# Performance work log

Hardware: AMD Instinct MI355X
Metric: run time of the kernel (lower is better)

The kernel has to match this reference:

```python
import jax, jax.numpy as jnp
import numpy as np

NC = 6            # CPAB tessellation cells (tess_size=6, zero_boundary=True)
DIM = NC - 1      # theta dimension = 5
SIG_LEN = 2048
CHANNELS = 3
BATCH = 256
FC_IN = 64 * 168  # flattened net_part1 output for signal_len=2048
NUM_SCALING = 0   # N in transform_data_ss
EPS_BN = 1e-5


def _cpab_basis():
    """QR null-space basis of the CPAB continuity + zero-boundary constraints.
    Params ordered [a_1,b_1,...,a_NC,b_NC]; v(x)=a_c x + b_c on cell c."""
    nc = NC
    L = np.zeros((nc + 1, 2 * nc))
    for k in range(1, nc):  # continuity at internal knots x_k = k/nc
        xk = k / nc
        L[k - 1, 2 * (k - 1)] = xk
        L[k - 1, 2 * (k - 1) + 1] = 1.0
        L[k - 1, 2 * k] = -xk
        L[k - 1, 2 * k + 1] = -1.0
    L[nc - 1, 1] = 1.0        # v(0) = 0  -> b_1 = 0
    L[nc, 2 * (nc - 1)] = 1.0  # v(1) = 0 -> a_nc + b_nc = 0
    L[nc, 2 * nc - 1] = 1.0
    Q, _ = np.linalg.qr(L.T, mode='complete')
    return np.ascontiguousarray(Q[:, nc + 1:]).astype(np.float32)  # (12, 5)


def _conv1d(x, w, b):
    y = jax.lax.conv_general_dilated(x, w, (1,), 'VALID',
                                     dimension_numbers=('NCH', 'OIH', 'NCH'))
    return y + b[None, :, None]


def _maxpool1d(x, k, s):
    return jax.lax.reduce_window(x, -jnp.inf, jax.lax.max, (1, 1, k), (1, 1, s), 'VALID')


def _bn(x, g, b, m, v):  # eval-mode BatchNorm1d
    return (x - m[None, :, None]) * (g / jnp.sqrt(v + EPS_BN))[None, :, None] + b[None, :, None]


def _integrate(x, A):
    """Exact CPAB 1D flow integration over t=1 with cell-crossing handling.
    x: (B, n) points in [0,1]; A: (B, NC, 2) per-cell (a, b). Monotone
    trajectories cross at most NC-1 boundaries -> fixed NC+1 iterations."""
    a_all, b_all = A[:, :, 0], A[:, :, 1]
    t = jnp.ones_like(x)
    for _ in range(NC + 1):
        c = jnp.clip(jnp.floor(x * NC).astype(jnp.int32), 0, NC - 1)
        a = jnp.take_along_axis(a_all, c, axis=1)
        b = jnp.take_along_axis(b_all, c, axis=1)
        v = a * x + b
        xb = jnp.where(v >= 0, (c + 1).astype(x.dtype) / NC, c.astype(x.dtype) / NC)
        big_a = jnp.abs(a) > 1e-8
        a_s = jnp.where(big_a, a, 1.0)
        z = x + b / a_s        # shifted coord: x(t) = z*exp(a t) - b/a
        zb = xb + b / a_s
        ratio = zb / jnp.where(jnp.abs(z) > 1e-12, z, 1e-12)
        t_exp = jnp.log(jnp.maximum(ratio, 1e-12)) / a_s
        v_s = jnp.where(jnp.abs(v) > 1e-12, v, 1.0)
        t_lin = (xb - x) / v_s
        thit = jnp.where(big_a, t_exp, t_lin)
        valid = (jnp.abs(v) > 1e-12) & (thit > 0) & (jnp.where(big_a, ratio, 1.0) > 0)
        thit = jnp.where(valid, thit, jnp.inf)
        tau = jnp.minimum(t, thit)
        x_new = jnp.where(big_a, z * jnp.exp(a * tau) - (z - x), x + b * tau)
        hit = thit <= t
        nudge = jnp.where(v >= 0, 1e-6, -1e-6)  # push into next cell
        x = jnp.clip(jnp.where(hit, xb + nudge, x_new), 0.0, 1.0)
        t = jnp.maximum(t - tau, 0.0)
    return x


def _interp1d(data, pos):
    """data: (B, L, C); pos: (B, n) in [0,1] -> (B, n, C) linear interpolation."""
    Lw = data.shape[1]
    p = jnp.clip(pos, 0.0, 1.0) * (Lw - 1)
    x0 = jnp.clip(jnp.floor(p).astype(jnp.int32), 0, Lw - 2)
    w = (p - x0.astype(p.dtype))[:, :, None]
    d0 = jnp.take_along_axis(data, x0[:, :, None], axis=1)
    d1 = jnp.take_along_axis(data, (x0 + 1)[:, :, None], axis=1)
    return d0 * (1.0 - w) + d1 * w


def _transform_data_ss(data, theta, basis, outsize, N):
    """CPAB scaling-and-squaring warp of data (B, L, C) by theta (B, DIM)."""
    Bsz = theta.shape[0]
    A = (theta @ basis.T).reshape(Bsz, NC, 2) / (2.0 ** N)
    grid = jnp.linspace(0.0, 1.0, outsize, dtype=data.dtype)
    grid_t = _integrate(jnp.broadcast_to(grid, (Bsz, outsize)), A)
    for _ in range(N):  # squaring: compose the warp with itself
        grid_t = _interp1d(grid_t[:, :, None], grid_t)[:, :, 0]
    return _interp1d(data, grid_t)


def reference(x, conv1_w, conv1_b, bn1_g, bn1_b, bn1_m, bn1_v,
              conv2_w, conv2_b, bn2_g, bn2_b, bn2_m, bn2_v,
              conv3_w, conv3_b, bn3_g, bn3_b, bn3_m, bn3_v,
              fc1_w, fc1_b, fc2_w, fc2_b, fc3_w, fc3_b, fc4_w, fc4_b, basis):
    # localization net (n_recurrence = 1, back_version = True)
    h = jax.nn.relu(_maxpool1d(_bn(_conv1d(x, conv1_w, conv1_b), bn1_g, bn1_b, bn1_m, bn1_v), 3, 2))
    h = jax.nn.relu(_maxpool1d(_bn(_conv1d(h, conv2_w, conv2_b), bn2_g, bn2_b, bn2_m, bn2_v), 3, 3))
    h = jax.nn.relu(_maxpool1d(_bn(_conv1d(h, conv3_w, conv3_b), bn3_g, bn3_b, bn3_m, bn3_v), 3, 2))
    xs = h.reshape(h.shape[0], -1)  # (B, 64*168)
    xs = jax.nn.relu(xs @ fc1_w.T + fc1_b)
    xs = jax.nn.relu(xs @ fc2_w.T + fc2_b)
    xs = jax.nn.relu(xs @ fc3_w.T + fc3_b)
    theta = jnp.tanh(xs @ fc4_w.T + fc4_b)  # (B, 5)
    data = jnp.transpose(x, (0, 2, 1))       # (B, L, C)
    warped = _transform_data_ss(data, theta, basis, SIG_LEN, NUM_SCALING)
    return jnp.transpose(warped, (0, 2, 1))  # (B, C, L)


def setup_inputs() -> dict:
    key = jax.random.key(0)
    ks = jax.random.split(key, 16)
    def nrm(k, shape, scale):
        return (jax.random.normal(k, shape) * scale).astype(jnp.float32)
    inp = {}
    inp['x'] = jax.random.normal(ks[0], (BATCH, CHANNELS, SIG_LEN), dtype=jnp.float32)
    inp['conv1_w'] = nrm(ks[1], (128, CHANNELS, 3), (CHANNELS * 3) ** -0.5)
    inp['conv1_b'] = nrm(ks[2], (128,), 0.01)
    inp['bn1_g'] = jnp.ones((128,), jnp.float32)
    inp['bn1_b'] = jnp.zeros((128,), jnp.float32)
    inp['bn1_m'] = nrm(ks[3], (128,), 0.1)
    inp['bn1_v'] = jnp.ones((128,), jnp.float32)
    inp['conv2_w'] = nrm(ks[4], (64, 128, 5), (128 * 5) ** -0.5)
    inp['conv2_b'] = nrm(ks[5], (64,), 0.01)
    inp['bn2_g'] = jnp.ones((64,), jnp.float32)
    inp['bn2_b'] = jnp.zeros((64,), jnp.float32)
    inp['bn2_m'] = nrm(ks[6], (64,), 0.1)
    inp['bn2_v'] = jnp.ones((64,), jnp.float32)
    inp['conv3_w'] = nrm(ks[7], (64, 64, 3), (64 * 3) ** -0.5)
    inp['conv3_b'] = nrm(ks[8], (64,), 0.01)
    inp['bn3_g'] = jnp.ones((64,), jnp.float32)
    inp['bn3_b'] = jnp.zeros((64,), jnp.float32)
    inp['bn3_m'] = nrm(ks[9], (64,), 0.1)
    inp['bn3_v'] = jnp.ones((64,), jnp.float32)
    inp['fc1_w'] = nrm(ks[10], (48, FC_IN), FC_IN ** -0.5)
    inp['fc1_b'] = jnp.zeros((48,), jnp.float32)
    inp['fc2_w'] = nrm(ks[11], (32, 48), 48 ** -0.5)
    inp['fc2_b'] = jnp.zeros((32,), jnp.float32)
    inp['fc3_w'] = nrm(ks[12], (16, 32), 32 ** -0.5)
    inp['fc3_b'] = jnp.zeros((16,), jnp.float32)
    # near-identity warp head (original zero-inits weight, identity bias)
    inp['fc4_w'] = nrm(ks[13], (DIM, 16), 0.01)
    inp['fc4_b'] = nrm(ks[14], (DIM,), 0.01)
    inp['basis'] = jnp.asarray(_cpab_basis())
    return inp
```

## Files before the change

kernel.cpp:

```cpp
#include <hip/hip_runtime.h>
#include <math.h>

#define BATCH   256
#define SIGLEN  2048
#define L1OUT   1022
#define L2OUT   339
#define L3OUT   168
#define FCIN    10752

#define TP2   16
#define NROW  52
#define H1S   136
#define H1SZ  (NROW*H1S)

#define TU3   28

typedef float f32x2  __attribute__((ext_vector_type(2)));
typedef float f32x4  __attribute__((ext_vector_type(4)));
typedef short s16x8  __attribute__((ext_vector_type(8)));

__device__ __forceinline__ unsigned short f2bf(float f) {
    unsigned int u = __float_as_uint(f);
    return (unsigned short)((u + 0x7fffu + ((u >> 16) & 1u)) >> 16);
}
__device__ __forceinline__ float bf2f(unsigned short h) {
    return __uint_as_float(((unsigned int)h) << 16);
}
__device__ __forceinline__ f32x2 pkfma(f32x2 a, f32x2 b, f32x2 c) {
    f32x2 d;
    asm("v_pk_fma_f32 %0, %1, %2, %3" : "=v"(d) : "v"(a), "v"(b), "v"(c));
    return d;
}

__launch_bounds__(256)
__global__ void prep_kernel(
    const float* __restrict__ conv1_b,
    const float* __restrict__ g1, const float* __restrict__ b1,
    const float* __restrict__ m1, const float* __restrict__ v1,
    const float* __restrict__ conv2_w, const float* __restrict__ conv2_b,
    const float* __restrict__ g2, const float* __restrict__ b2,
    const float* __restrict__ m2, const float* __restrict__ v2,
    const float* __restrict__ conv3_w, const float* __restrict__ conv3_b,
    const float* __restrict__ g3, const float* __restrict__ b3,
    const float* __restrict__ m3, const float* __restrict__ v3,
    const float* __restrict__ fc1_w,
    unsigned short* __restrict__ w2hi, unsigned short* __restrict__ w2lo,
    unsigned short* __restrict__ w3hi, unsigned short* __restrict__ w3lo,
    float* __restrict__ wp1,
    float* __restrict__ so1, float* __restrict__ so2, float* __restrict__ so3)
{
    __shared__ float tl[64 * 169];

    int t   = threadIdx.x;
    int tid = blockIdx.x * 256 + t;
    int stride = gridDim.x * 256;

    if (blockIdx.x < 48) {
        int o = blockIdx.x;
        for (int i = t; i < FCIN; i += 256) {
            int co = i / L3OUT, u = i - co * L3OUT;
            tl[co * 169 + u] = fc1_w[o * FCIN + i];
        }
        __syncthreads();
        for (int i = t; i < FCIN; i += 256) {
            int u = i >> 6, co = i & 63;
            wp1[o * FCIN + i] = tl[co * 169 + u];
        }
    }

    for (int i = tid; i < 64*128*5; i += stride) {
        int co = i / 640; int rr = i - co*640; int ci = rr / 5; int k = rr - ci*5;
        float w = conv2_w[i];
        unsigned short hi = f2bf(w);
        unsigned short lo = f2bf(w - bf2f(hi));
        int dst = ((k*4 + (ci >> 5))*64 + co)*32 + (ci & 31);
        w2hi[dst] = hi;
        w2lo[dst] = lo;
    }
    for (int i = tid; i < 64*64*3; i += stride) {
        int co = i / 192; int r = i - co*192; int ci = r / 3; int k = r - ci*3;
        float w = conv3_w[i];
        unsigned short hi = f2bf(w);
        unsigned short lo = f2bf(w - bf2f(hi));
        int dst = ((k*2 + (ci >> 5))*64 + co)*32 + (ci & 31);
        w3hi[dst] = hi;
        w3lo[dst] = lo;
    }
    if (tid < 128) {
        float s = g1[tid] / sqrtf(v1[tid] + 1e-5f);
        so1[tid]       = s;
        so1[128 + tid] = (conv1_b[tid] - m1[tid]) * s + b1[tid];
    }
    if (tid < 64) {
        float s2 = g2[tid] / sqrtf(v2[tid] + 1e-5f);
        so2[tid]      = s2;
        so2[64 + tid] = (conv2_b[tid] - m2[tid]) * s2 + b2[tid];
        float s3 = g3[tid] / sqrtf(v3[tid] + 1e-5f);
        so3[tid]      = s3;
        so3[64 + tid] = (conv3_b[tid] - m3[tid]) * s3 + b3[tid];
    }
}

__launch_bounds__(256, 5)
__global__ void conv12_kernel(
    const float* __restrict__ x, const float* __restrict__ w1,
    const unsigned short* __restrict__ w2hi, const unsigned short* __restrict__ w2lo,
    const float* __restrict__ so1, const float* __restrict__ so2,
    unsigned int* __restrict__ h2p)
{
    __shared__ unsigned short h1hi[H1SZ];
    __shared__ unsigned short h1lo[H1SZ];

    int t  = threadIdx.x;
    int b  = blockIdx.x;
    int u0 = blockIdx.y * TP2;
    int q0 = 3 * u0;
    int wv = __builtin_amdgcn_readfirstlane(t >> 6);
    int l  = t & 63;
    int m  = l & 15;
    int qd = l >> 4;

    {
        f32x2 wp[9], s1p, o1p;
        const float* wa = w1 + (2*l)*9;
        #pragma unroll
        for (int j = 0; j < 9; ++j) wp[j] = (f32x2){wa[j], wa[9 + j]};
        s1p = (f32x2){so1[2*l], so1[2*l + 1]};
        o1p = (f32x2){so1[128 + 2*l], so1[128 + 2*l + 1]};

        int rbase = 13 * wv;
        int W0 = 2*(q0 + rbase);
        const float* xp0 = x + b*3*SIGLEN;

        f32x2 xb[3][6];
        if (W0 + 5 <= SIGLEN - 1) {
            #pragma unroll
            for (int ci = 0; ci < 3; ++ci) {
                const float* xp = xp0 + ci*SIGLEN + W0;
                float2 v01 = *(const float2*)(xp);
                float2 v23 = *(const float2*)(xp + 2);
                float2 v45 = *(const float2*)(xp + 4);
                xb[ci][0] = (f32x2){v01.x, v01.x};
                xb[ci][1] = (f32x2){v01.y, v01.y};
                xb[ci][2] = (f32x2){v23.x, v23.x};
                xb[ci][3] = (f32x2){v23.y, v23.y};
                xb[ci][4] = (f32x2){v45.x, v45.x};
                xb[ci][5] = (f32x2){v45.y, v45.y};
            }
        } else {
            #pragma unroll
            for (int ci = 0; ci < 3; ++ci)
                #pragma unroll
                for (int j = 0; j < 6; ++j) {
                    int xi = W0 + j; xi = xi < SIGLEN ? xi : SIGLEN - 1;
                    float v = xp0[ci*SIGLEN + xi];
                    xb[ci][j] = (f32x2){v, v};
                }
        }

        f32x2 cr = (f32x2){0.f, 0.f};
        #pragma unroll
        for (int s = 0; s < 13; ++s) {
            int r = rbase + s;
            f32x2 r1 = (f32x2){0.f, 0.f}, r2 = (f32x2){0.f, 0.f};
            #pragma unroll
            for (int ci = 0; ci < 3; ++ci) {
                #pragma unroll
                for (int tp = 0; tp < 3; ++tp) {
                    r1 = pkfma(xb[ci][1 + tp], wp[ci*3 + tp], r1);
                    r2 = pkfma(xb[ci][2 + tp], wp[ci*3 + tp], r2);
                }
            }
            f32x2 r0;
            if (s == 0) {
                r0 = (f32x2){0.f, 0.f};
                #pragma unroll
                for (int ci = 0; ci < 3; ++ci)
                    #pragma unroll
                    for (int tp = 0; tp < 3; ++tp)
                        r0 = pkfma(xb[ci][tp], wp[ci*3 + tp], r0);
            } else {
                r0 = cr;
            }
            cr = r2;

            float m0 = fmaxf(r0[0], fmaxf(r1[0], r2[0]));
            float m1 = fmaxf(r0[1], fmaxf(r1[1], r2[1]));
            float v0 = fmaxf(fmaf(s1p[0], m0, o1p[0]), 0.f);
            float v1 = fmaxf(fmaf(s1p[1], m1, o1p[1]), 0.f);

            unsigned ua = __float_as_uint(v0);
            unsigned ub = __float_as_uint(v1);
            unsigned hipack = __builtin_amdgcn_perm(ub, ua, 0x07060302u);
            float ra = v0 - __uint_as_float(ua & 0xffff0000u);
            float rb = v1 - __uint_as_float(ub & 0xffff0000u);
            unsigned lopack = __builtin_amdgcn_perm(__float_as_uint(rb), __float_as_uint(ra),
                                                    0x07060302u);
            ((unsigned*)h1hi)[r*68 + l] = hipack;
            ((unsigned*)h1lo)[r*68 + l] = lopack;

            if (s < 12) {
                #pragma unroll
                for (int ci = 0; ci < 3; ++ci) {
                    xb[ci][0] = xb[ci][2]; xb[ci][1] = xb[ci][3];
                    xb[ci][2] = xb[ci][4]; xb[ci][3] = xb[ci][5];
                }
                int Wn = W0 + 2*s + 6;
                if (Wn + 1 <= SIGLEN - 1) {
                    #pragma unroll
                    for (int ci = 0; ci < 3; ++ci) {
                        float2 v = *(const float2*)(xp0 + ci*SIGLEN + Wn);
                        xb[ci][4] = (f32x2){v.x, v.x};
                        xb[ci][5] = (f32x2){v.y, v.y};
                    }
                } else {
                    #pragma unroll
                    for (int ci = 0; ci < 3; ++ci) {
                        int x4 = Wn     < SIGLEN ? Wn     : SIGLEN - 1;
                        int x5 = Wn + 1 < SIGLEN ? Wn + 1 : SIGLEN - 1;
                        float a4 = xp0[ci*SIGLEN + x4];
                        float a5 = xp0[ci*SIGLEN + x5];
                        xb[ci][4] = (f32x2){a4, a4};
                        xb[ci][5] = (f32x2){a5, a5};
                    }
                }
            }
        }
    }
    __syncthreads();

    f32x4 acc[3] = {(f32x4)(0.f), (f32x4)(0.f), (f32x4)(0.f)};

    const unsigned short* whb = w2hi + wv*512 + m*32 + qd*8;
    const unsigned short* wlb = w2lo + wv*512 + m*32 + qd*8;

    for (int k = 0; k < 5; ++k) {
        #pragma unroll
        for (int cb = 0; cb < 4; ++cb) {
            int st = k*4 + cb;
            s16x8 wh = *(const s16x8*)(whb + st*2048);
            s16x8 wl = *(const s16x8*)(wlb + st*2048);
            #pragma unroll
            for (int pt = 0; pt < 3; ++pt) {
                int row = pt*16 + m + k;
                s16x8 ah = *(const s16x8*)&h1hi[row*H1S + cb*32 + qd*8];
                s16x8 al = *(const s16x8*)&h1lo[row*H1S + cb*32 + qd*8];
                acc[pt] = __builtin_amdgcn_mfma_f32_16x16x32_bf16(ah, wh, acc[pt], 0, 0, 0);
                acc[pt] = __builtin_amdgcn_mfma_f32_16x16x32_bf16(al, wh, acc[pt], 0, 0, 0);
                acc[pt] = __builtin_amdgcn_mfma_f32_16x16x32_bf16(ah, wl, acc[pt], 0, 0, 0);
            }
        }
    }
    __syncthreads();

    float* c2 = (float*)h1hi;
    #pragma unroll
    for (int pt = 0; pt < 3; ++pt)
        #pragma unroll
        for (int rg = 0; rg < 4; ++rg)
            c2[(pt*16 + qd*4 + rg)*65 + wv*16 + m] = acc[pt][rg];
    __syncthreads();

    #pragma unroll
    for (int it = 0; it < 4; ++it) {
        int idx = t + it*256;
        int ul = idx >> 6, co = idx & 63;
        int u = u0 + ul;
        if (u < L2OUT) {
            float v0 = c2[(3*ul  )*65 + co];
            float v1 = c2[(3*ul+1)*65 + co];
            float v2 = c2[(3*ul+2)*65 + co];
            float mm = fmaxf(v0, fmaxf(v1, v2));
            float v  = fmaxf(fmaf(so2[co], mm, so2[64 + co]), 0.f);
            unsigned uu = __float_as_uint(v);
            float rr = v - __uint_as_float(uu & 0xffff0000u);
            h2p[(b*L2OUT + u)*64 + co] = (uu >> 16) | (__float_as_uint(rr) & 0xffff0000u);
        }
    }
}

__launch_bounds__(256, 4)
__global__ void conv3fc1_kernel(
    const unsigned int* __restrict__ h2p,
    const unsigned short* __restrict__ w3hi, const unsigned short* __restrict__ w3lo,
    const float* __restrict__ so3, const float* __restrict__ wp1,
    float* __restrict__ part)
{
    __shared__ unsigned short h3s[2*66*72];
    __shared__ float c3buf[64*65];

    int t  = threadIdx.x;
    int b  = blockIdx.x;
    int ti = blockIdx.y;
    int u0 = ti * TU3;
    int wv = __builtin_amdgcn_readfirstlane(t >> 6);
    int l  = t & 63;
    int m  = l & 15;
    int qd = l >> 4;

    for (int i = t; i < 66*64; i += 256) {
        int r = i >> 6, ci = i & 63;
        int g = 2*u0 + r; g = g > (L2OUT-1) ? (L2OUT-1) : g;
        unsigned int v = h2p[(b*L2OUT + g)*64 + ci];
        h3s[r*72 + ci]         = (unsigned short)(v & 0xffffu);
        h3s[66*72 + r*72 + ci] = (unsigned short)(v >> 16);
    }
    __syncthreads();

    s16x8 wh[6], wl[6];
    #pragma unroll
    for (int s = 0; s < 6; ++s) {
        wh[s] = *(const s16x8*)(w3hi + s*2048 + (wv*16 + m)*32 + qd*8);
        wl[s] = *(const s16x8*)(w3lo + s*2048 + (wv*16 + m)*32 + qd*8);
    }

    f32x4 acc[4] = {(f32x4)(0.f), (f32x4)(0.f), (f32x4)(0.f), (f32x4)(0.f)};
    #pragma unroll
    for (int pt = 0; pt < 4; ++pt) {
        #pragma unroll
        for (int s = 0; s < 6; ++s) {
            int row = pt*16 + m + (s >> 1);
            int off = (s & 1)*32 + qd*8;
            s16x8 ah = *(const s16x8*)&h3s[row*72 + off];
            s16x8 al = *(const s16x8*)&h3s[66*72 + row*72 + off];
            acc[pt] = __builtin_amdgcn_mfma_f32_16x16x32_bf16(ah, wh[s], acc[pt], 0, 0, 0);
            acc[pt] = __builtin_amdgcn_mfma_f32_16x16x32_bf16(al, wh[s], acc[pt], 0, 0, 0);
            acc[pt] = __builtin_amdgcn_mfma_f32_16x16x32_bf16(ah, wl[s], acc[pt], 0, 0, 0);
        }
    }
    __syncthreads();

    #pragma unroll
    for (int pt = 0; pt < 4; ++pt)
        #pragma unroll
        for (int rg = 0; rg < 4; ++rg)
            c3buf[(pt*16 + qd*4 + rg)*65 + wv*16 + m] = acc[pt][rg];
    __syncthreads();

    float s3 = so3[l], o3 = so3[64 + l];
    float pooled[TU3];
    #pragma unroll
    for (int u = 0; u < TU3; ++u) {
        int p = 2*u;
        float v0 = c3buf[(p  )*65 + l];
        float v1 = c3buf[(p+1)*65 + l];
        float v2 = c3buf[(p+2)*65 + l];
        pooled[u] = fmaxf(fmaf(s3, fmaxf(v0, fmaxf(v1, v2)), o3), 0.f);
    }

    int o0 = wv * 12;
    float fa[12];
    #pragma unroll
    for (int j = 0; j < 12; ++j) fa[j] = 0.f;
    #pragma unroll 4
    for (int u = 0; u < TU3; ++u) {
        float pv = pooled[u];
        const float* wp = wp1 + (u0 + u)*64 + l;
        #pragma unroll
        for (int j = 0; j < 12; ++j)
            fa[j] = fmaf(pv, wp[(o0 + j)*FCIN], fa[j]);
    }
    #pragma unroll
    for (int j = 0; j < 12; ++j) {
        #pragma unroll
        for (int off = 32; off > 0; off >>= 1)
            fa[j] += __shfl_xor(fa[j], off, 64);
    }
    if (l == 0) {
        #pragma unroll
        for (int j = 0; j < 12; ++j)
            part[(b*6 + ti)*48 + o0 + j] = fa[j];
    }
}

__launch_bounds__(256)
__global__ void warp_kernel(
    const float* __restrict__ x, const float* __restrict__ part,
    const float* __restrict__ fc1_b,
    const float* __restrict__ fc2_w, const float* __restrict__ fc2_b,
    const float* __restrict__ fc3_w, const float* __restrict__ fc3_b,
    const float* __restrict__ fc4_w, const float* __restrict__ fc4_b,
    const float* __restrict__ basis,
    float* __restrict__ out)
{
    __shared__ float xs48[48], hl[32], gl[16], thl[5], Al[12];

    int b = blockIdx.x;
    int t = threadIdx.x;

    if (t < 48) {
        float sv = 0.f;
        #pragma unroll
        for (int ti = 0; ti < 6; ++ti) sv += part[(b*6 + ti)*48 + t];
        xs48[t] = fmaxf(sv + fc1_b[t], 0.f);
    }
    __syncthreads();
    if (t < 32) {
        float sv = fc2_b[t];
        #pragma unroll
        for (int k = 0; k < 48; ++k) sv = fmaf(fc2_w[t * 48 + k], xs48[k], sv);
        hl[t] = fmaxf(sv, 0.f);
    }
    __syncthreads();
    if (t < 16) {
        float sv = fc3_b[t];
        #pragma unroll
        for (int k = 0; k < 32; ++k) sv = fmaf(fc3_w[t * 32 + k], hl[k], sv);
        gl[t] = fmaxf(sv, 0.f);
    }
    __syncthreads();
    if (t < 5) {
        float sv = fc4_b[t];
        #pragma unroll
        for (int k = 0; k < 16; ++k) sv = fmaf(fc4_w[t * 16 + k], gl[k], sv);
        thl[t] = tanhf(sv);
    }
    __syncthreads();
    if (t < 12) {
        float sv = 0.f;
        #pragma unroll
        for (int d = 0; d < 5; ++d) sv = fmaf(basis[t * 5 + d], thl[d], sv);
        Al[t] = sv;
    }
    __syncthreads();

    float a_r[6], b_r[6];
    #pragma unroll
    for (int c = 0; c < 6; ++c) { a_r[c] = Al[2*c]; b_r[c] = Al[2*c+1]; }

    #pragma unroll
    for (int cc = 0; cc < 2; ++cc) {
        int i = (blockIdx.y * 2 + cc) * 256 + t;
        float xp = (float)i / 2047.f;
        float tt = 1.f;
        for (int it = 0; it < 7; ++it) {
            int c = (int)floorf(xp * 6.f);
            c = min(max(c, 0), 5);
            float a  = a_r[c], bb = b_r[c];
            float v  = a * xp + bb;
            float xb = (v >= 0.f) ? (float)(c + 1) / 6.f : (float)c / 6.f;
            bool  big_a = fabsf(a) > 1e-8f;
            float a_s = big_a ? a : 1.f;
            float z   = xp + bb / a_s;
            float zb  = xb + bb / a_s;
            float zden = (fabsf(z) > 1e-12f) ? z : 1e-12f;
            float ratio = zb / zden;
            float t_exp = logf(fmaxf(ratio, 1e-12f)) / a_s;
            float v_s   = (fabsf(v) > 1e-12f) ? v : 1.f;
            float t_lin = (xb - xp) / v_s;
            float thit  = big_a ? t_exp : t_lin;
            bool valid  = (fabsf(v) > 1e-12f) && (thit > 0.f) && ((big_a ? ratio : 1.f) > 0.f);
            if (!valid) thit = __builtin_inff();
            float tau   = fminf(tt, thit);
            float x_new = big_a ? (z * expf(a * tau) - (z - xp)) : (xp + bb * tau);
            bool hit    = (thit <= tt);
            float nudge = (v >= 0.f) ? 1e-6f : -1e-6f;
            xp = hit ? (xb + nudge) : x_new;
            xp = fminf(fmaxf(xp, 0.f), 1.f);
            tt = fmaxf(tt - tau, 0.f);
        }
        float p = fminf(fmaxf(xp, 0.f), 1.f) * 2047.f;
        int i0 = (int)floorf(p);
        i0 = min(max(i0, 0), 2046);
        float w = p - (float)i0;
        #pragma unroll
        for (int c = 0; c < 3; ++c) {
            const float* d = &x[(b * 3 + c) * SIGLEN];
            out[(b * 3 + c) * SIGLEN + i] = d[i0] * (1.f - w) + d[i0 + 1] * w;
        }
    }
}

extern "C" void kernel_launch(void* const* d_in, const int* in_sizes, int n_in,
                              void* d_out, int out_size, void* d_ws, size_t ws_size,
                              hipStream_t stream) {
    (void)in_sizes; (void)n_in; (void)out_size; (void)ws_size;
    const float* x       = (const float*)d_in[0];
    const float* conv1_w = (const float*)d_in[1];
    const float* conv1_b = (const float*)d_in[2];
    const float* bn1_g   = (const float*)d_in[3];
    const float* bn1_b   = (const float*)d_in[4];
    const float* bn1_m   = (const float*)d_in[5];
    const float* bn1_v   = (const float*)d_in[6];
    const float* conv2_w = (const float*)d_in[7];
    const float* conv2_b = (const float*)d_in[8];
    const float* bn2_g   = (const float*)d_in[9];
    const float* bn2_b   = (const float*)d_in[10];
    const float* bn2_m   = (const float*)d_in[11];
    const float* bn2_v   = (const float*)d_in[12];
    const float* conv3_w = (const float*)d_in[13];
    const float* conv3_b = (const float*)d_in[14];
    const float* bn3_g   = (const float*)d_in[15];
    const float* bn3_b   = (const float*)d_in[16];
    const float* bn3_m   = (const float*)d_in[17];
    const float* bn3_v   = (const float*)d_in[18];
    const float* fc1_w   = (const float*)d_in[19];
    const float* fc1_b   = (const float*)d_in[20];
    const float* fc2_w   = (const float*)d_in[21];
    const float* fc2_b   = (const float*)d_in[22];
    const float* fc3_w   = (const float*)d_in[23];
    const float* fc3_b   = (const float*)d_in[24];
    const float* fc4_w   = (const float*)d_in[25];
    const float* fc4_b   = (const float*)d_in[26];
    const float* basis   = (const float*)d_in[27];

    unsigned short* w2hi = (unsigned short*)d_ws;
    unsigned short* w2lo = w2hi + 40960;
    unsigned short* w3hi = w2lo + 40960;
    unsigned short* w3lo = w3hi + 12288;
    float* ws   = (float*)d_ws;
    float* so1  = ws + 53248;
    float* so2  = so1 + 256;
    float* so3  = so2 + 128;
    float* wp1  = so3 + 128;
    unsigned int* h2p = (unsigned int*)(wp1 + 516096);
    float* part = (float*)(h2p + 5554176);

    prep_kernel<<<128, 256, 0, stream>>>(
        conv1_b, bn1_g, bn1_b, bn1_m, bn1_v,
        conv2_w, conv2_b, bn2_g, bn2_b, bn2_m, bn2_v,
        conv3_w, conv3_b, bn3_g, bn3_b, bn3_m, bn3_v,
        fc1_w, w2hi, w2lo, w3hi, w3lo, wp1, so1, so2, so3);

    dim3 g2(BATCH, (L2OUT + TP2 - 1) / TP2);
    conv12_kernel<<<g2, 256, 0, stream>>>(x, conv1_w, w2hi, w2lo, so1, so2, h2p);

    dim3 g3(BATCH, 6);
    conv3fc1_kernel<<<g3, 256, 0, stream>>>(h2p, w3hi, w3lo, so3, wp1, part);

    dim3 g5(BATCH, 4);
    warp_kernel<<<g5, 256, 0, stream>>>(x, part, fc1_b, fc2_w, fc2_b,
                                        fc3_w, fc3_b, fc4_w, fc4_b, basis,
                                        (float*)d_out);
}
```

Baseline: 242.2 us.

## Fuse conv3+fc1 and warp kernels into a single per-batch tail kernel

Merges the conv3/pool/fc1 partial kernel and the MLP+CPAB warp kernel into one 512-thread block per batch item. The whole h2 slice is staged once in LDS and looped over six tiles, and fc1 is reduced in-block instead of through a global partial buffer. This removes one launch and the partial-sum round trip. In exchange the grid shrinks from 1536+1024 blocks to 256 large blocks with about 120KB of LDS each, which lowers occupancy and parallelism.

```diff
diff --git a/kernel.cpp b/kernel.cpp
--- a/kernel.cpp
+++ b/kernel.cpp
@@ -13,7 +13,7 @@
 #define H1S   136
 #define H1SZ  (NROW*H1S)
 
-#define TU3   28
+#define H3R   346
 
 typedef float f32x2  __attribute__((ext_vector_type(2)));
 typedef float f32x4  __attribute__((ext_vector_type(4)));
@@ -279,121 +279,110 @@
     }
 }
 
-__launch_bounds__(256, 4)
-__global__ void conv3fc1_kernel(
+__launch_bounds__(512, 1)
+__global__ void tail_kernel(
     const unsigned int* __restrict__ h2p,
     const unsigned short* __restrict__ w3hi, const unsigned short* __restrict__ w3lo,
     const float* __restrict__ so3, const float* __restrict__ wp1,
-    float* __restrict__ part)
-{
-    __shared__ unsigned short h3s[2*66*72];
-    __shared__ float c3buf[64*65];
-
-    int t  = threadIdx.x;
-    int b  = blockIdx.x;
-    int ti = blockIdx.y;
-    int u0 = ti * TU3;
-    int wv = __builtin_amdgcn_readfirstlane(t >> 6);
-    int l  = t & 63;
-    int m  = l & 15;
-    int qd = l >> 4;
-
-    for (int i = t; i < 66*64; i += 256) {
-        int r = i >> 6, ci = i & 63;
-        int g = 2*u0 + r; g = g > (L2OUT-1) ? (L2OUT-1) : g;
-        unsigned int v = h2p[(b*L2OUT + g)*64 + ci];
-        h3s[r*72 + ci]         = (unsigned short)(v & 0xffffu);
-        h3s[66*72 + r*72 + ci] = (unsigned short)(v >> 16);
-    }
-    __syncthreads();
-
-    s16x8 wh[6], wl[6];
-    #pragma unroll
-    for (int s = 0; s < 6; ++s) {
-        wh[s] = *(const s16x8*)(w3hi + s*2048 + (wv*16 + m)*32 + qd*8);
-        wl[s] = *(const s16x8*)(w3lo + s*2048 + (wv*16 + m)*32 + qd*8);
-    }
-
-    f32x4 acc[4] = {(f32x4)(0.f), (f32x4)(0.f), (f32x4)(0.f), (f32x4)(0.f)};
-    #pragma unroll
-    for (int pt = 0; pt < 4; ++pt) {
-        #pragma unroll
-        for (int s = 0; s < 6; ++s) {
-            int row = pt*16 + m + (s >> 1);
-            int off = (s & 1)*32 + qd*8;
-            s16x8 ah = *(const s16x8*)&h3s[row*72 + off];
-            s16x8 al = *(const s16x8*)&h3s[66*72 + row*72 + off];
-            acc[pt] = __builtin_amdgcn_mfma_f32_16x16x32_bf16(ah, wh[s], acc[pt], 0, 0, 0);
-            acc[pt] = __builtin_amdgcn_mfma_f32_16x16x32_bf16(al, wh[s], acc[pt], 0, 0, 0);
-            acc[pt] = __builtin_amdgcn_mfma_f32_16x16x32_bf16(ah, wl[s], acc[pt], 0, 0, 0);
-        }
-    }
-    __syncthreads();
-
-    #pragma unroll
-    for (int pt = 0; pt < 4; ++pt)
-        #pragma unroll
-        for (int rg = 0; rg < 4; ++rg)
-            c3buf[(pt*16 + qd*4 + rg)*65 + wv*16 + m] = acc[pt][rg];
-    __syncthreads();
-
-    float s3 = so3[l], o3 = so3[64 + l];
-    float pooled[TU3];
-    #pragma unroll
-    for (int u = 0; u < TU3; ++u) {
-        int p = 2*u;
-        float v0 = c3buf[(p  )*65 + l];
-        float v1 = c3buf[(p+1)*65 + l];
-        float v2 = c3buf[(p+2)*65 + l];
-        pooled[u] = fmaxf(fmaf(s3, fmaxf(v0, fmaxf(v1, v2)), o3), 0.f);
-    }
-
-    int o0 = wv * 12;
-    float fa[12];
-    #pragma unroll
-    for (int j = 0; j < 12; ++j) fa[j] = 0.f;
-    #pragma unroll 4
-    for (int u = 0; u < TU3; ++u) {
-        float pv = pooled[u];
-        const float* wp = wp1 + (u0 + u)*64 + l;
-        #pragma unroll
-        for (int j = 0; j < 12; ++j)
-            fa[j] = fmaf(pv, wp[(o0 + j)*FCIN], fa[j]);
-    }
-    #pragma unroll
-    for (int j = 0; j < 12; ++j) {
-        #pragma unroll
-        for (int off = 32; off > 0; off >>= 1)
-            fa[j] += __shfl_xor(fa[j], off, 64);
-    }
-    if (l == 0) {
-        #pragma unroll
-        for (int j = 0; j < 12; ++j)
-            part[(b*6 + ti)*48 + o0 + j] = fa[j];
-    }
-}
-
-__launch_bounds__(256)
-__global__ void warp_kernel(
-    const float* __restrict__ x, const float* __restrict__ part,
     const float* __restrict__ fc1_b,
     const float* __restrict__ fc2_w, const float* __restrict__ fc2_b,
     const float* __restrict__ fc3_w, const float* __restrict__ fc3_b,
     const float* __restrict__ fc4_w, const float* __restrict__ fc4_b,
     const float* __restrict__ basis,
+    const float* __restrict__ x,
     float* __restrict__ out)
 {
+    __shared__ unsigned short h3s[2*H3R*72];
+    __shared__ float c3buf[64*65];
+    __shared__ float xsr[48];
     __shared__ float xs48[48], hl[32], gl[16], thl[5], Al[12];
 
-    int b = blockIdx.x;
-    int t = threadIdx.x;
-
-    if (t < 48) {
-        float sv = 0.f;
-        #pragma unroll
-        for (int ti = 0; ti < 6; ++ti) sv += part[(b*6 + ti)*48 + t];
-        xs48[t] = fmaxf(sv + fc1_b[t], 0.f);
-    }
+    int t  = threadIdx.x;
+    int b  = blockIdx.x;
+    int wv = __builtin_amdgcn_readfirstlane(t >> 6);
+    int l  = t & 63;
+    int m  = l & 15;
+    int qd = l >> 4;
+    int hh = wv >> 2;
+    int c4 = wv & 3;
+
+    for (int i = t; i < H3R*64; i += 512) {
+        int r = i >> 6, ci = i & 63;
+        int g = r > (L2OUT-1) ? (L2OUT-1) : r;
+        unsigned int v = h2p[(b*L2OUT + g)*64 + ci];
+        h3s[r*72 + ci]           = (unsigned short)(v & 0xffffu);
+        h3s[H3R*72 + r*72 + ci]  = (unsigned short)(v >> 16);
+    }
+
+    s16x8 wh[6], wl[6];
+    #pragma unroll
+    for (int s = 0; s < 6; ++s) {
+        wh[s] = *(const s16x8*)(w3hi + s*2048 + (c4*16 + m)*32 + qd*8);
+        wl[s] = *(const s16x8*)(w3lo + s*2048 + (c4*16 + m)*32 + qd*8);
+    }
+    float s3 = so3[l], o3 = so3[64 + l];
+
+    __syncthreads();
+
+    int o0 = wv * 6;
+    float fa[6];
+    #pragma unroll
+    for (int j = 0; j < 6; ++j) fa[j] = 0.f;
+
+    for (int ti = 0; ti < 6; ++ti) {
+        int u0 = ti * 28;
+
+        f32x4 acc[2] = {(f32x4)(0.f), (f32x4)(0.f)};
+        #pragma unroll
+        for (int pp = 0; pp < 2; ++pp) {
+            int pt = 2*hh + pp;
+            #pragma unroll
+            for (int s = 0; s < 6; ++s) {
+                int row = 2*u0 + pt*16 + m + (s >> 1);
+                int off = (s & 1)*32 + qd*8;
+                s16x8 ah = *(const s16x8*)&h3s[row*72 + off];
+                s16x8 al = *(const s16x8*)&h3s[H3R*72 + row*72 + off];
+                acc[pp] = __builtin_amdgcn_mfma_f32_16x16x32_bf16(ah, wh[s], acc[pp], 0, 0, 0);
+                acc[pp] = __builtin_amdgcn_mfma_f32_16x16x32_bf16(al, wh[s], acc[pp], 0, 0, 0);
+                acc[pp] = __builtin_amdgcn_mfma_f32_16x16x32_bf16(ah, wl[s], acc[pp], 0, 0, 0);
+            }
+        }
+        __syncthreads();
+
+        #pragma unroll
+        for (int pp = 0; pp < 2; ++pp)
+            #pragma unroll
+            for (int rg = 0; rg < 4; ++rg)
+                c3buf[((2*hh + pp)*16 + qd*4 + rg)*65 + c4*16 + m] = acc[pp][rg];
+        __syncthreads();
+
+        #pragma unroll 4
+        for (int u = 0; u < 28; ++u) {
+            int p = 2*u;
+            float v0 = c3buf[(p  )*65 + l];
+            float v1 = c3buf[(p+1)*65 + l];
+            float v2 = c3buf[(p+2)*65 + l];
+            float pv = fmaxf(fmaf(s3, fmaxf(v0, fmaxf(v1, v2)), o3), 0.f);
+            const float* wp = wp1 + (u0 + u)*64 + l;
+            #pragma unroll
+            for (int j = 0; j < 6; ++j)
+                fa[j] = fmaf(pv, wp[(o0 + j)*FCIN], fa[j]);
+        }
+    }
+
+    #pragma unroll
+    for (int j = 0; j < 6; ++j) {
+        #pragma unroll
+        for (int off = 32; off > 0; off >>= 1)
+            fa[j] += __shfl_xor(fa[j], off, 64);
+    }
+    if (l == 0) {
+        #pragma unroll
+        for (int j = 0; j < 6; ++j) xsr[o0 + j] = fa[j];
+    }
+    __syncthreads();
+
+    if (t < 48) xs48[t] = fmaxf(xsr[t] + fc1_b[t], 0.f);
     __syncthreads();
     if (t < 32) {
         float sv = fc2_b[t];
@@ -429,8 +418,8 @@
     for (int c = 0; c < 6; ++c) { a_r[c] = Al[2*c]; b_r[c] = Al[2*c+1]; }
 
     #pragma unroll
-    for (int cc = 0; cc < 2; ++cc) {
-        int i = (blockIdx.y * 2 + cc) * 256 + t;
+    for (int cc = 0; cc < 4; ++cc) {
+        int i = cc * 512 + t;
         float xp = (float)i / 2047.f;
         float tt = 1.f;
         for (int it = 0; it < 7; ++it) {
@@ -514,7 +503,6 @@
     float* so3  = so2 + 128;
     float* wp1  = so3 + 128;
     unsigned int* h2p = (unsigned int*)(wp1 + 516096);
-    float* part = (float*)(h2p + 5554176);
 
     prep_kernel<<<128, 256, 0, stream>>>(
         conv1_b, bn1_g, bn1_b, bn1_m, bn1_v,
@@ -525,11 +513,7 @@
     dim3 g2(BATCH, (L2OUT + TP2 - 1) / TP2);
     conv12_kernel<<<g2, 256, 0, stream>>>(x, conv1_w, w2hi, w2lo, so1, so2, h2p);
 
-    dim3 g3(BATCH, 6);
-    conv3fc1_kernel<<<g3, 256, 0, stream>>>(h2p, w3hi, w3lo, so3, wp1, part);
-
-    dim3 g5(BATCH, 4);
-    warp_kernel<<<g5, 256, 0, stream>>>(x, part, fc1_b, fc2_w, fc2_b,
-                                        fc3_w, fc3_b, fc4_w, fc4_b, basis,
-                                        (float*)d_out);
-}
+    tail_kernel<<<BATCH, 512, 0, stream>>>(h2p, w3hi, w3lo, so3, wp1,
+                                           fc1_b, fc2_w, fc2_b, fc3_w, fc3_b,
+                                           fc4_w, fc4_b, basis, x, (float*)d_out);
+}
```

New measurement: 242.8 us. About the same (+0.2%).
